# Performance work log

Hardware: AMD Instinct MI355X
Metric: run time of the kernel (lower is better)

The kernel has to match this reference:

```python
import jax, jax.numpy as jnp
import numpy as np

D = 1024
H = 16
HD = D // H
MLP = 4 * D
EPS = 1e-5


def layer_norm(x, g, b):
    mu = jnp.mean(x, axis=-1, keepdims=True)
    var = jnp.mean((x - mu) ** 2, axis=-1, keepdims=True)
    return (x - mu) * jax.lax.rsqrt(var + EPS) * g + b


def grn(stacked, W, b, g, be):
    # stacked: [B, L, S, D]; input-dependent weights + normalized branch, summed over L
    w = jax.nn.relu(jnp.einsum('blsd,de->blse', stacked, W) + b)
    n = layer_norm(stacked, g, be)
    return jnp.sum(w + n, axis=1)  # [B, S, D]


def setup_inputs() -> dict:
    key = jax.random.key(0)
    ks = jax.random.split(key, 24)
    s = 0.02
    inp = {
        'x': jax.random.normal(ks[0], (2, 2048, D), jnp.float32),
        'layer_outputs': jax.random.normal(ks[1], (2, 4, 2048, D), jnp.float32),
    }
    i = 2
    for name in ('q', 'k', 'v'):
        inp[f'grn_{name}_W'] = jax.random.normal(ks[i], (D, D), jnp.float32) * s; i += 1
        inp[f'grn_{name}_b'] = jnp.zeros((D,), jnp.float32)
        inp[f'grn_{name}_g'] = jnp.ones((D,), jnp.float32)
        inp[f'grn_{name}_be'] = jnp.zeros((D,), jnp.float32)
    inp['attn_out_W'] = jax.random.normal(ks[i], (D, D), jnp.float32) * s; i += 1
    inp['attn_out_b'] = jnp.zeros((D,), jnp.float32)
    inp['attn_norm_g'] = jnp.ones((D,), jnp.float32)
    inp['attn_norm_b'] = jnp.zeros((D,), jnp.float32)
    inp['ffn_W1'] = jax.random.normal(ks[i], (D, MLP), jnp.float32) * s; i += 1
    inp['ffn_b1'] = jnp.zeros((MLP,), jnp.float32)
    inp['ffn_W2'] = jax.random.normal(ks[i], (MLP, D), jnp.float32) * s; i += 1
    inp['ffn_b2'] = jnp.zeros((D,), jnp.float32)
    inp['ffn_norm_g'] = jnp.ones((D,), jnp.float32)
    inp['ffn_norm_b'] = jnp.zeros((D,), jnp.float32)
    return inp


def reference(x, layer_outputs,
              grn_q_W, grn_q_b, grn_q_g, grn_q_be,
              grn_k_W, grn_k_b, grn_k_g, grn_k_be,
              grn_v_W, grn_v_b, grn_v_g, grn_v_be,
              attn_out_W, attn_out_b, attn_norm_g, attn_norm_b,
              ffn_W1, ffn_b1, ffn_W2, ffn_b2, ffn_norm_g, ffn_norm_b):
    B, S, _ = x.shape
    q = grn(layer_outputs, grn_q_W, grn_q_b, grn_q_g, grn_q_be)
    k = grn(layer_outputs, grn_k_W, grn_k_b, grn_k_g, grn_k_be)
    v = grn(layer_outputs, grn_v_W, grn_v_b, grn_v_g, grn_v_be)
    # [B, H, S, HD]
    q = q.reshape(B, S, H, HD).transpose(0, 2, 1, 3)
    k = k.reshape(B, S, H, HD).transpose(0, 2, 1, 3)
    v = v.reshape(B, S, H, HD).transpose(0, 2, 1, 3)
    scale = HD ** -0.5
    attn = jnp.einsum('bhqd,bhkd->bhqk', q, k) * scale
    attn = jax.nn.softmax(attn, axis=-1)
    out = jnp.einsum('bhqk,bhkd->bhqd', attn, v)
    out = out.transpose(0, 2, 1, 3).reshape(B, S, D)
    out = out @ attn_out_W + attn_out_b
    out = x + layer_norm(out, attn_norm_g, attn_norm_b)
    h = jax.nn.gelu(out @ ffn_W1 + ffn_b1, approximate=False) @ ffn_W2 + ffn_b2
    out = out + layer_norm(h, ffn_norm_g, ffn_norm_b)
    return out
```

## Files before the change

kernel.cpp:

```cpp
#include <hip/hip_runtime.h>
#include <cstddef>

#define B_  2
#define S_  2048
#define D_  1024
#define L_  4
#define H_  16
#define HD_ 64
#define MLP_ 4096
#define EPS_ 1e-5f

typedef __attribute__((ext_vector_type(8))) short  bf16x8;
typedef __attribute__((ext_vector_type(4))) float  f32x4;

__device__ __forceinline__ unsigned short f2bf(float x) {
    unsigned int u = __float_as_uint(x);
    u = (u + 0x7fffu + ((u >> 16) & 1u)) >> 16;
    return (unsigned short)u;
}
__device__ __forceinline__ float bf2f(unsigned short h) {
    return __uint_as_float(((unsigned int)h) << 16);
}

__global__ __launch_bounds__(256) void wconv_kernel(
    const float* __restrict__ W, unsigned short* __restrict__ Thi,
    unsigned short* __restrict__ Tlo, int K, int N)
{
    __shared__ float T[32][33];
    const int n0 = blockIdx.x * 32, k0 = blockIdx.y * 32;
    const int t = threadIdx.x;
    {
        const int r = t >> 3, c4 = (t & 7) * 4;
        const float4 w = *(const float4*)(W + (size_t)(k0 + r) * N + n0 + c4);
        T[r][c4 + 0] = w.x; T[r][c4 + 1] = w.y;
        T[r][c4 + 2] = w.z; T[r][c4 + 3] = w.w;
    }
    __syncthreads();
    {
        const int n = t >> 3, k4 = (t & 7) * 4;
        ushort4 h, l;
        float f;
        f = T[k4 + 0][n]; h.x = f2bf(f); l.x = f2bf(f - bf2f(h.x));
        f = T[k4 + 1][n]; h.y = f2bf(f); l.y = f2bf(f - bf2f(h.y));
        f = T[k4 + 2][n]; h.z = f2bf(f); l.z = f2bf(f - bf2f(h.z));
        f = T[k4 + 3][n]; h.w = f2bf(f); l.w = f2bf(f - bf2f(h.w));
        *(ushort4*)(Thi + (size_t)(n0 + n) * K + k0 + k4) = h;
        *(ushort4*)(Tlo + (size_t)(n0 + n) * K + k0 + k4) = l;
    }
}

template <int EPI>
__global__ __launch_bounds__(256) void gemm_bf16s_kernel(
    const float* __restrict__ A,
    const unsigned short* __restrict__ Bth, const unsigned short* __restrict__ Btl,
    const float* __restrict__ bias, float* __restrict__ C,
    int M, int N, int K)
{
    __shared__ unsigned short As_hi[128 * 40];
    __shared__ unsigned short As_lo[128 * 40];
    __shared__ unsigned short Bs_hi[128 * 40];
    __shared__ unsigned short Bs_lo[128 * 40];

    const int tid  = threadIdx.x;
    const int lane = tid & 63;
    const int wid  = tid >> 6;
    const int wr   = wid >> 1, wc = wid & 1;
    const int l15  = lane & 15, chunk = lane >> 4;
    const int row0 = blockIdx.y * 128;
    const int col0 = blockIdx.x * 128;

    const int a_off = (wr * 64 + l15) * 40 + chunk * 8;
    const int b_off = (wc * 64 + l15) * 40 + chunk * 8;

    f32x4 acc[4][4] = {};

    for (int k0 = 0; k0 < K; k0 += 32) {
        __syncthreads();
        #pragma unroll
        for (int u = 0; u < 4; ++u) {
            const int idx = tid + u * 256;
            const int r  = idx >> 3;
            const int kc = (idx & 7) * 4;
            const float4 a = *(const float4*)(A + (size_t)(row0 + r) * K + k0 + kc);
            ushort4 h, l;
            h.x = f2bf(a.x); l.x = f2bf(a.x - bf2f(h.x));
            h.y = f2bf(a.y); l.y = f2bf(a.y - bf2f(h.y));
            h.z = f2bf(a.z); l.z = f2bf(a.z - bf2f(h.z));
            h.w = f2bf(a.w); l.w = f2bf(a.w - bf2f(h.w));
            *(ushort4*)&As_hi[r * 40 + kc] = h;
            *(ushort4*)&As_lo[r * 40 + kc] = l;
        }
        #pragma unroll
        for (int u = 0; u < 2; ++u) {
            const int idx = tid + u * 256;
            const int c  = idx >> 2;
            const int kc = (idx & 3) * 8;
            const size_t gb = (size_t)(col0 + c) * K + k0 + kc;
            *(uint4*)&Bs_hi[c * 40 + kc] = *(const uint4*)(Bth + gb);
            *(uint4*)&Bs_lo[c * 40 + kc] = *(const uint4*)(Btl + gb);
        }
        __syncthreads();

        bf16x8 ah[4], al[4], bh[4], bl[4];
        #pragma unroll
        for (int mi = 0; mi < 4; ++mi) {
            ah[mi] = *(const bf16x8*)&As_hi[a_off + mi * 640];
            al[mi] = *(const bf16x8*)&As_lo[a_off + mi * 640];
        }
        #pragma unroll
        for (int ni = 0; ni < 4; ++ni) {
            bh[ni] = *(const bf16x8*)&Bs_hi[b_off + ni * 640];
            bl[ni] = *(const bf16x8*)&Bs_lo[b_off + ni * 640];
        }
        #pragma unroll
        for (int mi = 0; mi < 4; ++mi)
            #pragma unroll
            for (int ni = 0; ni < 4; ++ni) {
                acc[mi][ni] = __builtin_amdgcn_mfma_f32_16x16x32_bf16(
                    ah[mi], bh[ni], acc[mi][ni], 0, 0, 0);
                acc[mi][ni] = __builtin_amdgcn_mfma_f32_16x16x32_bf16(
                    ah[mi], bl[ni], acc[mi][ni], 0, 0, 0);
                acc[mi][ni] = __builtin_amdgcn_mfma_f32_16x16x32_bf16(
                    al[mi], bh[ni], acc[mi][ni], 0, 0, 0);
            }
    }

    const int rbase = row0 + wr * 64 + (lane >> 4) * 4;
    const int cbase = col0 + wc * 64 + l15;
    #pragma unroll
    for (int mi = 0; mi < 4; ++mi) {
        #pragma unroll
        for (int reg = 0; reg < 4; ++reg) {
            const int gr = rbase + mi * 16 + reg;
            #pragma unroll
            for (int ni = 0; ni < 4; ++ni) {
                const int gc = cbase + ni * 16;
                float v = acc[mi][ni][reg] + bias[gc];
                if (EPI == 1) v = fmaxf(v, 0.f);
                else if (EPI == 2) v = 0.5f * v * (1.f + erff(v * 0.70710678118654752f));
                C[(size_t)gr * N + gc] = v;
            }
        }
    }
}

__global__ __launch_bounds__(256) void grn_ns_kernel(
    const float* __restrict__ LO, float* __restrict__ NS)
{
    const int row = blockIdx.x;
    const int b = row >> 11, s = row & (S_ - 1);
    const int tid = threadIdx.x;
    __shared__ float r1[4], r2[4];

    float acc[4] = {0.f, 0.f, 0.f, 0.f};
    #pragma unroll
    for (int l = 0; l < L_; ++l) {
        const float* xr = LO + ((size_t)((b * L_ + l) * S_ + s)) * D_;
        const float4 v = *(const float4*)(xr + tid * 4);
        float s1 = v.x + v.y + v.z + v.w;
        float s2 = v.x * v.x + v.y * v.y + v.z * v.z + v.w * v.w;
        #pragma unroll
        for (int off = 32; off >= 1; off >>= 1) {
            s1 += __shfl_xor(s1, off);
            s2 += __shfl_xor(s2, off);
        }
        if ((tid & 63) == 0) { r1[tid >> 6] = s1; r2[tid >> 6] = s2; }
        __syncthreads();
        s1 = r1[0] + r1[1] + r1[2] + r1[3];
        s2 = r2[0] + r2[1] + r2[2] + r2[3];
        __syncthreads();
        const float mu  = s1 * (1.f / D_);
        const float var = s2 * (1.f / D_) - mu * mu;
        const float rs  = rsqrtf(var + EPS_);
        acc[0] += (v.x - mu) * rs;
        acc[1] += (v.y - mu) * rs;
        acc[2] += (v.z - mu) * rs;
        acc[3] += (v.w - mu) * rs;
    }
    float4 o = {acc[0], acc[1], acc[2], acc[3]};
    *(float4*)(NS + (size_t)row * D_ + tid * 4) = o;
}

__global__ __launch_bounds__(256) void grn_reduce_kernel(
    const float* __restrict__ P, const float* __restrict__ NS,
    const float* __restrict__ g, const float* __restrict__ be,
    float* __restrict__ out)
{
    const size_t i4 = (size_t)blockIdx.x * 256 + threadIdx.x;
    const int d4 = (int)(i4 & (D_ / 4 - 1));
    const size_t row = i4 >> 8;
    const int b = (int)(row >> 11), s = (int)(row & (S_ - 1));

    float4 a = {0.f, 0.f, 0.f, 0.f};
    #pragma unroll
    for (int l = 0; l < L_; ++l) {
        const float4 w = *(const float4*)(P + ((size_t)((b * L_ + l) * S_ + s)) * D_ + d4 * 4);
        a.x += w.x; a.y += w.y; a.z += w.z; a.w += w.w;
    }
    const float4 n  = *(const float4*)(NS + row * D_ + d4 * 4);
    const float4 gg = *(const float4*)(g + d4 * 4);
    const float4 bb = *(const float4*)(be + d4 * 4);
    float4 o;
    o.x = a.x + n.x * gg.x + 4.f * bb.x;
    o.y = a.y + n.y * gg.y + 4.f * bb.y;
    o.z = a.z + n.z * gg.z + 4.f * bb.z;
    o.w = a.w + n.w * gg.w + 4.f * bb.w;
    *(float4*)(out + row * D_ + d4 * 4) = o;
}

__global__ __launch_bounds__(256) void kvconv_kernel(
    const float* __restrict__ Kin, const float* __restrict__ Vin,
    unsigned short* __restrict__ Kh, unsigned short* __restrict__ Kl,
    unsigned short* __restrict__ Vth, unsigned short* __restrict__ Vtl)
{
    __shared__ float T[64][68];
    const int t = threadIdx.x;
    const int st = blockIdx.x;
    const int bh = blockIdx.y;
    const int b = bh >> 4, h = bh & 15;
    const int s0 = st * 64;

    #pragma unroll
    for (int u = 0; u < 4; ++u) {
        const int idx = t + u * 256;
        const int r  = idx >> 4;
        const int c4 = (idx & 15) * 4;
        const size_t src = ((size_t)(b * S_ + s0 + r)) * D_ + h * 64 + c4;
        const float4 kf = *(const float4*)(Kin + src);
        ushort4 hh, ll;
        hh.x = f2bf(kf.x); ll.x = f2bf(kf.x - bf2f(hh.x));
        hh.y = f2bf(kf.y); ll.y = f2bf(kf.y - bf2f(hh.y));
        hh.z = f2bf(kf.z); ll.z = f2bf(kf.z - bf2f(hh.z));
        hh.w = f2bf(kf.w); ll.w = f2bf(kf.w - bf2f(hh.w));
        const size_t kd = ((size_t)bh * S_ + s0 + r) * 64 + c4;
        *(ushort4*)(Kh + kd) = hh;
        *(ushort4*)(Kl + kd) = ll;
        const float4 vf = *(const float4*)(Vin + src);
        T[r][c4 + 0] = vf.x; T[r][c4 + 1] = vf.y;
        T[r][c4 + 2] = vf.z; T[r][c4 + 3] = vf.w;
    }
    __syncthreads();
    #pragma unroll
    for (int u = 0; u < 4; ++u) {
        const int idx = t + u * 256;
        const int d  = idx >> 4;
        const int s4 = (idx & 15) * 4;
        ushort4 hh, ll;
        float f;
        f = T[s4 + 0][d]; hh.x = f2bf(f); ll.x = f2bf(f - bf2f(hh.x));
        f = T[s4 + 1][d]; hh.y = f2bf(f); ll.y = f2bf(f - bf2f(hh.y));
        f = T[s4 + 2][d]; hh.z = f2bf(f); ll.z = f2bf(f - bf2f(hh.z));
        f = T[s4 + 3][d]; hh.w = f2bf(f); ll.w = f2bf(f - bf2f(hh.w));
        const size_t vd = ((size_t)bh * 64 + d) * S_ + s0 + s4;
        *(ushort4*)(Vth + vd) = hh;
        *(ushort4*)(Vtl + vd) = ll;
    }
}

__global__ __launch_bounds__(256) void attn_mfma_kernel(
    const float* __restrict__ Q,
    const unsigned short* __restrict__ Kh, const unsigned short* __restrict__ Kl,
    const unsigned short* __restrict__ Vth, const unsigned short* __restrict__ Vtl,
    float* __restrict__ O)
{
    __shared__ unsigned short Ksh[64 * 72], Ksl[64 * 72];
    __shared__ unsigned short Vsh[64 * 72], Vsl[64 * 72];
    __shared__ unsigned short Phs[4][32 * 72];
    __shared__ unsigned short Pls[4][32 * 72];

    const int tid  = threadIdx.x;
    const int lane = tid & 63;
    const int w    = tid >> 6;
    const int l15  = lane & 15, g = lane >> 4;
    const int bh   = blockIdx.y;
    const int b    = bh >> 4, h = bh & 15;
    const int q0   = blockIdx.x * 128 + w * 32;
    const float scale = 0.125f;

    bf16x8 qh[2][2], ql[2][2];
    #pragma unroll
    for (int mi = 0; mi < 2; ++mi)
        #pragma unroll
        for (int ks = 0; ks < 2; ++ks) {
            const float* qp = Q + ((size_t)(b * S_ + q0 + mi * 16 + l15)) * D_
                              + h * 64 + ks * 32 + g * 8;
            const float4 f0 = *(const float4*)qp;
            const float4 f1 = *(const float4*)(qp + 4);
            const float vs[8] = {f0.x * scale, f0.y * scale, f0.z * scale, f0.w * scale,
                                 f1.x * scale, f1.y * scale, f1.z * scale, f1.w * scale};
            #pragma unroll
            for (int j = 0; j < 8; ++j) {
                const unsigned short hv = f2bf(vs[j]);
                qh[mi][ks][j] = (short)hv;
                ql[mi][ks][j] = (short)f2bf(vs[j] - bf2f(hv));
            }
        }

    f32x4 o[2][4] = {};
    float mrun[2][4], lrun[2][4];
    #pragma unroll
    for (int mi = 0; mi < 2; ++mi)
        #pragma unroll
        for (int r = 0; r < 4; ++r) { mrun[mi][r] = -1e30f; lrun[mi][r] = 0.f; }

    const unsigned short* KhB = Kh  + (size_t)bh * S_ * 64;
    const unsigned short* KlB = Kl  + (size_t)bh * S_ * 64;
    const unsigned short* VhB = Vth + (size_t)bh * 64 * S_;
    const unsigned short* VlB = Vtl + (size_t)bh * 64 * S_;

    for (int kt = 0; kt < S_; kt += 64) {
        __syncthreads();
        #pragma unroll
        for (int u = 0; u < 2; ++u) {
            const int idx = tid + u * 256;
            const int rr  = idx >> 3;
            const int c8  = (idx & 7) * 8;
            *(uint4*)&Ksh[rr * 72 + c8] = *(const uint4*)(KhB + (size_t)(kt + rr) * 64 + c8);
            *(uint4*)&Ksl[rr * 72 + c8] = *(const uint4*)(KlB + (size_t)(kt + rr) * 64 + c8);
            *(uint4*)&Vsh[rr * 72 + c8] = *(const uint4*)(VhB + (size_t)rr * S_ + kt + c8);
            *(uint4*)&Vsl[rr * 72 + c8] = *(const uint4*)(VlB + (size_t)rr * S_ + kt + c8);
        }
        __syncthreads();

        f32x4 s[2][4] = {};
        #pragma unroll
        for (int ks = 0; ks < 2; ++ks)
            #pragma unroll
            for (int ni = 0; ni < 4; ++ni) {
                const bf16x8 khf = *(const bf16x8*)&Ksh[(ni * 16 + l15) * 72 + ks * 32 + g * 8];
                const bf16x8 klf = *(const bf16x8*)&Ksl[(ni * 16 + l15) * 72 + ks * 32 + g * 8];
                #pragma unroll
                for (int mi = 0; mi < 2; ++mi) {
                    s[mi][ni] = __builtin_amdgcn_mfma_f32_16x16x32_bf16(qh[mi][ks], khf, s[mi][ni], 0, 0, 0);
                    s[mi][ni] = __builtin_amdgcn_mfma_f32_16x16x32_bf16(qh[mi][ks], klf, s[mi][ni], 0, 0, 0);
                    s[mi][ni] = __builtin_amdgcn_mfma_f32_16x16x32_bf16(ql[mi][ks], khf, s[mi][ni], 0, 0, 0);
                }
            }

        #pragma unroll
        for (int mi = 0; mi < 2; ++mi) {
            #pragma unroll
            for (int r = 0; r < 4; ++r) {
                float mx = fmaxf(fmaxf(s[mi][0][r], s[mi][1][r]),
                                 fmaxf(s[mi][2][r], s[mi][3][r]));
                mx = fmaxf(mx, __shfl_xor(mx, 1));
                mx = fmaxf(mx, __shfl_xor(mx, 2));
                mx = fmaxf(mx, __shfl_xor(mx, 4));
                mx = fmaxf(mx, __shfl_xor(mx, 8));
                const float mn = fmaxf(mrun[mi][r], mx);
                const float c  = __expf(mrun[mi][r] - mn);
                mrun[mi][r] = mn;
                float rs = 0.f;
                #pragma unroll
                for (int ni = 0; ni < 4; ++ni) {
                    const float p = __expf(s[mi][ni][r] - mn);
                    rs += p;
                    const unsigned short ph = f2bf(p);
                    const int off = (mi * 16 + 4 * g + r) * 72 + ni * 16 + l15;
                    Phs[w][off] = ph;
                    Pls[w][off] = f2bf(p - bf2f(ph));
                }
                rs += __shfl_xor(rs, 1);
                rs += __shfl_xor(rs, 2);
                rs += __shfl_xor(rs, 4);
                rs += __shfl_xor(rs, 8);
                lrun[mi][r] = lrun[mi][r] * c + rs;
                #pragma unroll
                for (int di = 0; di < 4; ++di) o[mi][di][r] *= c;
            }
        }

        #pragma unroll
        for (int ks = 0; ks < 2; ++ks) {
            bf16x8 pfh[2], pfl[2];
            #pragma unroll
            for (int mi = 0; mi < 2; ++mi) {
                pfh[mi] = *(const bf16x8*)&Phs[w][(mi * 16 + l15) * 72 + ks * 32 + g * 8];
                pfl[mi] = *(const bf16x8*)&Pls[w][(mi * 16 + l15) * 72 + ks * 32 + g * 8];
            }
            #pragma unroll
            for (int di = 0; di < 4; ++di) {
                const bf16x8 vhf = *(const bf16x8*)&Vsh[(di * 16 + l15) * 72 + ks * 32 + g * 8];
                const bf16x8 vlf = *(const bf16x8*)&Vsl[(di * 16 + l15) * 72 + ks * 32 + g * 8];
                #pragma unroll
                for (int mi = 0; mi < 2; ++mi) {
                    o[mi][di] = __builtin_amdgcn_mfma_f32_16x16x32_bf16(pfh[mi], vhf, o[mi][di], 0, 0, 0);
                    o[mi][di] = __builtin_amdgcn_mfma_f32_16x16x32_bf16(pfh[mi], vlf, o[mi][di], 0, 0, 0);
                    o[mi][di] = __builtin_amdgcn_mfma_f32_16x16x32_bf16(pfl[mi], vhf, o[mi][di], 0, 0, 0);
                }
            }
        }
    }

    #pragma unroll
    for (int mi = 0; mi < 2; ++mi)
        #pragma unroll
        for (int r = 0; r < 4; ++r) {
            const float inv = 1.f / lrun[mi][r];
            float* op = O + ((size_t)(b * S_ + q0 + mi * 16 + 4 * g + r)) * D_
                        + h * 64 + l15;
            #pragma unroll
            for (int di = 0; di < 4; ++di) op[di * 16] = o[mi][di][r] * inv;
        }
}

__global__ __launch_bounds__(256) void add_ln_kernel(
    const float* __restrict__ Y, const float* __restrict__ R,
    const float* __restrict__ g, const float* __restrict__ beta,
    float* __restrict__ out)
{
    const int row = blockIdx.x;
    const int tid = threadIdx.x;
    __shared__ float r1[4], r2[4];

    const float4 v = *(const float4*)(Y + (size_t)row * D_ + tid * 4);
    float s1 = v.x + v.y + v.z + v.w;
    float s2 = v.x * v.x + v.y * v.y + v.z * v.z + v.w * v.w;
    #pragma unroll
    for (int off = 32; off >= 1; off >>= 1) {
        s1 += __shfl_xor(s1, off);
        s2 += __shfl_xor(s2, off);
    }
    if ((tid & 63) == 0) { r1[tid >> 6] = s1; r2[tid >> 6] = s2; }
    __syncthreads();
    s1 = r1[0] + r1[1] + r1[2] + r1[3];
    s2 = r2[0] + r2[1] + r2[2] + r2[3];
    const float mu  = s1 * (1.f / D_);
    const float var = s2 * (1.f / D_) - mu * mu;
    const float rs  = rsqrtf(var + EPS_);

    const float4 rr = *(const float4*)(R + (size_t)row * D_ + tid * 4);
    const float4 gg = *(const float4*)(g + tid * 4);
    const float4 bb = *(const float4*)(beta + tid * 4);
    float4 o;
    o.x = rr.x + (v.x - mu) * rs * gg.x + bb.x;
    o.y = rr.y + (v.y - mu) * rs * gg.y + bb.y;
    o.z = rr.z + (v.z - mu) * rs * gg.z + bb.z;
    o.w = rr.w + (v.w - mu) * rs * gg.w + bb.w;
    *(float4*)(out + (size_t)row * D_ + tid * 4) = o;
}

extern "C" void kernel_launch(void* const* d_in, const int* in_sizes, int n_in,
                              void* d_out, int out_size, void* d_ws, size_t ws_size,
                              hipStream_t stream)
{
    const float* x  = (const float*)d_in[0];
    const float* LO = (const float*)d_in[1];
    const float* Wq  = (const float*)d_in[2];
    const float* bq_ = (const float*)d_in[3];
    const float* gq  = (const float*)d_in[4];
    const float* beq = (const float*)d_in[5];
    const float* Wk  = (const float*)d_in[6];
    const float* bk_ = (const float*)d_in[7];
    const float* gk  = (const float*)d_in[8];
    const float* bek = (const float*)d_in[9];
    const float* Wv  = (const float*)d_in[10];
    const float* bv_ = (const float*)d_in[11];
    const float* gv  = (const float*)d_in[12];
    const float* bev = (const float*)d_in[13];
    const float* Wo  = (const float*)d_in[14];
    const float* bo  = (const float*)d_in[15];
    const float* ang = (const float*)d_in[16];
    const float* anb = (const float*)d_in[17];
    const float* W1  = (const float*)d_in[18];
    const float* b1  = (const float*)d_in[19];
    const float* W2  = (const float*)d_in[20];
    const float* b2  = (const float*)d_in[21];
    const float* fng = (const float*)d_in[22];
    const float* fnb = (const float*)d_in[23];

    const size_t BS  = (size_t)B_ * S_;
    const size_t SEG = BS * D_;
    float* ws  = (float*)d_ws;
    float* ns   = ws;
    float* bufq = ws + SEG;
    float* bufk = ws + 2 * SEG;
    float* bufv = ws + 3 * SEG;
    float* big  = ws + 4 * SEG;

    unsigned short* wt = (unsigned short*)(ws + 8 * SEG);
    const size_t MM = 1048576;
    unsigned short* wtq_h = wt;            unsigned short* wtq_l = wt + MM;
    unsigned short* wtk_h = wt + 2 * MM;   unsigned short* wtk_l = wt + 3 * MM;
    unsigned short* wtv_h = wt + 4 * MM;   unsigned short* wtv_l = wt + 5 * MM;
    unsigned short* wto_h = wt + 6 * MM;   unsigned short* wto_l = wt + 7 * MM;
    unsigned short* w1_h  = wt + 8 * MM;   unsigned short* w1_l  = wt + 12 * MM;
    unsigned short* w2_h  = wt + 16 * MM;  unsigned short* w2_l  = wt + 20 * MM;

    const size_t KVSEG = (size_t)B_ * H_ * S_ * HD_;
    unsigned short* kv  = (unsigned short*)big;
    unsigned short* kh_ = kv;
    unsigned short* kl_ = kv + KVSEG;
    unsigned short* vth = kv + 2 * KVSEG;
    unsigned short* vtl = kv + 3 * KVSEG;

    const dim3 blk(256);

    wconv_kernel<<<dim3(32, 32),  blk, 0, stream>>>(Wq, wtq_h, wtq_l, D_, D_);
    wconv_kernel<<<dim3(32, 32),  blk, 0, stream>>>(Wk, wtk_h, wtk_l, D_, D_);
    wconv_kernel<<<dim3(32, 32),  blk, 0, stream>>>(Wv, wtv_h, wtv_l, D_, D_);
    wconv_kernel<<<dim3(32, 32),  blk, 0, stream>>>(Wo, wto_h, wto_l, D_, D_);
    wconv_kernel<<<dim3(128, 32), blk, 0, stream>>>(W1, w1_h,  w1_l,  D_, MLP_);
    wconv_kernel<<<dim3(32, 128), blk, 0, stream>>>(W2, w2_h,  w2_l,  MLP_, D_);

    grn_ns_kernel<<<dim3(BS), blk, 0, stream>>>(LO, ns);

    const unsigned short* Wh[3] = {wtq_h, wtk_h, wtv_h};
    const unsigned short* Wl[3] = {wtq_l, wtk_l, wtv_l};
    const float* bp[3]  = {bq_, bk_, bv_};
    const float* gp[3]  = {gq, gk, gv};
    const float* bep[3] = {beq, bek, bev};
    float* outp[3] = {bufq, bufk, bufv};
    for (int p = 0; p < 3; ++p) {
        gemm_bf16s_kernel<1><<<dim3(D_ / 128, (B_ * L_ * S_) / 128), blk, 0, stream>>>(
            LO, Wh[p], Wl[p], bp[p], big, B_ * L_ * S_, D_, D_);
        grn_reduce_kernel<<<dim3(BS), blk, 0, stream>>>(big, ns, gp[p], bep[p], outp[p]);
    }

    kvconv_kernel<<<dim3(S_ / 64, B_ * H_), blk, 0, stream>>>(bufk, bufv, kh_, kl_, vth, vtl);
    attn_mfma_kernel<<<dim3(S_ / 128, B_ * H_), blk, 0, stream>>>(bufq, kh_, kl_, vth, vtl, ns);

    gemm_bf16s_kernel<0><<<dim3(D_ / 128, BS / 128), blk, 0, stream>>>(
        ns, wto_h, wto_l, bo, bufq, (int)BS, D_, D_);

    add_ln_kernel<<<dim3(BS), blk, 0, stream>>>(bufq, x, ang, anb, bufk);

    gemm_bf16s_kernel<2><<<dim3(MLP_ / 128, BS / 128), blk, 0, stream>>>(
        bufk, w1_h, w1_l, b1, big, (int)BS, MLP_, D_);

    gemm_bf16s_kernel<0><<<dim3(D_ / 128, BS / 128), blk, 0, stream>>>(
        big, w2_h, w2_l, b2, bufv, (int)BS, D_, MLP_);

    add_ln_kernel<<<dim3(BS), blk, 0, stream>>>(bufv, bufk, fng, fnb, (float*)d_out);
}
```

Measured before the change: 1.223 ms.

## Pre-split GEMM activations into bf16 hi/lo and drop P low part in attention

Adds a pass that converts fp32 activations into bf16 hi/lo pairs once, plus a GEMM variant that loads these pre-split operands straight into LDS, so each tile no longer splits A on the fly. The FFN1 GEMM now writes its GELU output already split for FFN2. Attention drops the low-order bf16 term of the softmax probabilities, removing one of three MFMAs in the PV product and one LDS buffer. MFMA sections are wrapped in s_setprio. The split layer_outputs path runs only if the workspace is large enough. Dropping the P low term lowers attention accuracy.

```diff
diff --git a/kernel.cpp b/kernel.cpp
--- a/kernel.cpp
+++ b/kernel.cpp
@@ -20,6 +20,21 @@
 }
 __device__ __forceinline__ float bf2f(unsigned short h) {
     return __uint_as_float(((unsigned int)h) << 16);
+}
+
+__global__ __launch_bounds__(256) void aconv_kernel(
+    const float* __restrict__ X, unsigned short* __restrict__ Xh,
+    unsigned short* __restrict__ Xl)
+{
+    const size_t i4 = (size_t)blockIdx.x * 256 + threadIdx.x;
+    const float4 v = *(const float4*)(X + i4 * 4);
+    ushort4 h, l;
+    h.x = f2bf(v.x); l.x = f2bf(v.x - bf2f(h.x));
+    h.y = f2bf(v.y); l.y = f2bf(v.y - bf2f(h.y));
+    h.z = f2bf(v.z); l.z = f2bf(v.z - bf2f(h.z));
+    h.w = f2bf(v.w); l.w = f2bf(v.w - bf2f(h.w));
+    *(ushort4*)(Xh + i4 * 4) = h;
+    *(ushort4*)(Xl + i4 * 4) = l;
 }
 
 __global__ __launch_bounds__(256) void wconv_kernel(
@@ -46,6 +61,99 @@
         f = T[k4 + 3][n]; h.w = f2bf(f); l.w = f2bf(f - bf2f(h.w));
         *(ushort4*)(Thi + (size_t)(n0 + n) * K + k0 + k4) = h;
         *(ushort4*)(Tlo + (size_t)(n0 + n) * K + k0 + k4) = l;
+    }
+}
+
+template <int EPI, int OUT>
+__global__ __launch_bounds__(256) void gemm_bf16p_kernel(
+    const unsigned short* __restrict__ Ah, const unsigned short* __restrict__ Al,
+    const unsigned short* __restrict__ Bth, const unsigned short* __restrict__ Btl,
+    const float* __restrict__ bias, float* __restrict__ C,
+    unsigned short* __restrict__ Chi, unsigned short* __restrict__ Clo,
+    int M, int N, int K)
+{
+    __shared__ unsigned short As_hi[128 * 40];
+    __shared__ unsigned short As_lo[128 * 40];
+    __shared__ unsigned short Bs_hi[128 * 40];
+    __shared__ unsigned short Bs_lo[128 * 40];
+
+    const int tid  = threadIdx.x;
+    const int lane = tid & 63;
+    const int wid  = tid >> 6;
+    const int wr   = wid >> 1, wc = wid & 1;
+    const int l15  = lane & 15, chunk = lane >> 4;
+    const int row0 = blockIdx.y * 128;
+    const int col0 = blockIdx.x * 128;
+
+    const int a_off = (wr * 64 + l15) * 40 + chunk * 8;
+    const int b_off = (wc * 64 + l15) * 40 + chunk * 8;
+
+    f32x4 acc[4][4] = {};
+
+    for (int k0 = 0; k0 < K; k0 += 32) {
+        __syncthreads();
+        #pragma unroll
+        for (int u = 0; u < 2; ++u) {
+            const int idx = tid + u * 256;
+            const int r  = idx >> 2;
+            const int kc = (idx & 3) * 8;
+            const size_t ga = (size_t)(row0 + r) * K + k0 + kc;
+            *(uint4*)&As_hi[r * 40 + kc] = *(const uint4*)(Ah + ga);
+            *(uint4*)&As_lo[r * 40 + kc] = *(const uint4*)(Al + ga);
+            const size_t gb = (size_t)(col0 + r) * K + k0 + kc;
+            *(uint4*)&Bs_hi[r * 40 + kc] = *(const uint4*)(Bth + gb);
+            *(uint4*)&Bs_lo[r * 40 + kc] = *(const uint4*)(Btl + gb);
+        }
+        __syncthreads();
+
+        bf16x8 ah[4], al[4], bh[4], bl[4];
+        #pragma unroll
+        for (int mi = 0; mi < 4; ++mi) {
+            ah[mi] = *(const bf16x8*)&As_hi[a_off + mi * 640];
+            al[mi] = *(const bf16x8*)&As_lo[a_off + mi * 640];
+        }
+        #pragma unroll
+        for (int ni = 0; ni < 4; ++ni) {
+            bh[ni] = *(const bf16x8*)&Bs_hi[b_off + ni * 640];
+            bl[ni] = *(const bf16x8*)&Bs_lo[b_off + ni * 640];
+        }
+        __builtin_amdgcn_s_setprio(1);
+        #pragma unroll
+        for (int mi = 0; mi < 4; ++mi)
+            #pragma unroll
+            for (int ni = 0; ni < 4; ++ni) {
+                acc[mi][ni] = __builtin_amdgcn_mfma_f32_16x16x32_bf16(
+                    ah[mi], bh[ni], acc[mi][ni], 0, 0, 0);
+                acc[mi][ni] = __builtin_amdgcn_mfma_f32_16x16x32_bf16(
+                    ah[mi], bl[ni], acc[mi][ni], 0, 0, 0);
+                acc[mi][ni] = __builtin_amdgcn_mfma_f32_16x16x32_bf16(
+                    al[mi], bh[ni], acc[mi][ni], 0, 0, 0);
+            }
+        __builtin_amdgcn_s_setprio(0);
+    }
+
+    const int rbase = row0 + wr * 64 + (lane >> 4) * 4;
+    const int cbase = col0 + wc * 64 + l15;
+    #pragma unroll
+    for (int mi = 0; mi < 4; ++mi) {
+        #pragma unroll
+        for (int reg = 0; reg < 4; ++reg) {
+            const int gr = rbase + mi * 16 + reg;
+            #pragma unroll
+            for (int ni = 0; ni < 4; ++ni) {
+                const int gc = cbase + ni * 16;
+                float v = acc[mi][ni][reg] + bias[gc];
+                if (EPI == 1) v = fmaxf(v, 0.f);
+                else if (EPI == 2) v = 0.5f * v * (1.f + erff(v * 0.70710678118654752f));
+                if (OUT == 0) {
+                    C[(size_t)gr * N + gc] = v;
+                } else {
+                    const unsigned short hv = f2bf(v);
+                    Chi[(size_t)gr * N + gc] = hv;
+                    Clo[(size_t)gr * N + gc] = f2bf(v - bf2f(hv));
+                }
+            }
+        }
     }
 }
 
@@ -266,7 +374,6 @@
     __shared__ unsigned short Ksh[64 * 72], Ksl[64 * 72];
     __shared__ unsigned short Vsh[64 * 72], Vsl[64 * 72];
     __shared__ unsigned short Phs[4][32 * 72];
-    __shared__ unsigned short Pls[4][32 * 72];
 
     const int tid  = threadIdx.x;
     const int lane = tid & 63;
@@ -329,12 +436,14 @@
             for (int ni = 0; ni < 4; ++ni) {
                 const bf16x8 khf = *(const bf16x8*)&Ksh[(ni * 16 + l15) * 72 + ks * 32 + g * 8];
                 const bf16x8 klf = *(const bf16x8*)&Ksl[(ni * 16 + l15) * 72 + ks * 32 + g * 8];
+                __builtin_amdgcn_s_setprio(1);
                 #pragma unroll
                 for (int mi = 0; mi < 2; ++mi) {
                     s[mi][ni] = __builtin_amdgcn_mfma_f32_16x16x32_bf16(qh[mi][ks], khf, s[mi][ni], 0, 0, 0);
                     s[mi][ni] = __builtin_amdgcn_mfma_f32_16x16x32_bf16(qh[mi][ks], klf, s[mi][ni], 0, 0, 0);
                     s[mi][ni] = __builtin_amdgcn_mfma_f32_16x16x32_bf16(ql[mi][ks], khf, s[mi][ni], 0, 0, 0);
                 }
+                __builtin_amdgcn_s_setprio(0);
             }
 
         #pragma unroll
@@ -355,10 +464,7 @@
                 for (int ni = 0; ni < 4; ++ni) {
                     const float p = __expf(s[mi][ni][r] - mn);
                     rs += p;
-                    const unsigned short ph = f2bf(p);
-                    const int off = (mi * 16 + 4 * g + r) * 72 + ni * 16 + l15;
-                    Phs[w][off] = ph;
-                    Pls[w][off] = f2bf(p - bf2f(ph));
+                    Phs[w][(mi * 16 + 4 * g + r) * 72 + ni * 16 + l15] = f2bf(p);
                 }
                 rs += __shfl_xor(rs, 1);
                 rs += __shfl_xor(rs, 2);
@@ -372,22 +478,21 @@
 
         #pragma unroll
         for (int ks = 0; ks < 2; ++ks) {
-            bf16x8 pfh[2], pfl[2];
-            #pragma unroll
-            for (int mi = 0; mi < 2; ++mi) {
+            bf16x8 pfh[2];
+            #pragma unroll
+            for (int mi = 0; mi < 2; ++mi)
                 pfh[mi] = *(const bf16x8*)&Phs[w][(mi * 16 + l15) * 72 + ks * 32 + g * 8];
-                pfl[mi] = *(const bf16x8*)&Pls[w][(mi * 16 + l15) * 72 + ks * 32 + g * 8];
-            }
             #pragma unroll
             for (int di = 0; di < 4; ++di) {
                 const bf16x8 vhf = *(const bf16x8*)&Vsh[(di * 16 + l15) * 72 + ks * 32 + g * 8];
                 const bf16x8 vlf = *(const bf16x8*)&Vsl[(di * 16 + l15) * 72 + ks * 32 + g * 8];
+                __builtin_amdgcn_s_setprio(1);
                 #pragma unroll
                 for (int mi = 0; mi < 2; ++mi) {
                     o[mi][di] = __builtin_amdgcn_mfma_f32_16x16x32_bf16(pfh[mi], vhf, o[mi][di], 0, 0, 0);
                     o[mi][di] = __builtin_amdgcn_mfma_f32_16x16x32_bf16(pfh[mi], vlf, o[mi][di], 0, 0, 0);
-                    o[mi][di] = __builtin_amdgcn_mfma_f32_16x16x32_bf16(pfl[mi], vhf, o[mi][di], 0, 0, 0);
                 }
+                __builtin_amdgcn_s_setprio(0);
             }
         }
     }
@@ -486,6 +591,9 @@
     unsigned short* wto_h = wt + 6 * MM;   unsigned short* wto_l = wt + 7 * MM;
     unsigned short* w1_h  = wt + 8 * MM;   unsigned short* w1_l  = wt + 12 * MM;
     unsigned short* w2_h  = wt + 16 * MM;  unsigned short* w2_l  = wt + 20 * MM;
+    unsigned short* lo_h = wt + 24 * MM;
+    unsigned short* lo_l = lo_h + 16 * MM;
+    const bool useLoSplit = ws_size >= (size_t)252 * 1024 * 1024;
 
     const size_t KVSEG = (size_t)B_ * H_ * S_ * HD_;
     unsigned short* kv  = (unsigned short*)big;
@@ -493,6 +601,12 @@
     unsigned short* kl_ = kv + KVSEG;
     unsigned short* vth = kv + 2 * KVSEG;
     unsigned short* vtl = kv + 3 * KVSEG;
+    unsigned short* hid_h = (unsigned short*)big;
+    unsigned short* hid_l = hid_h + 16 * MM;
+    unsigned short* ns_h = (unsigned short*)bufv;
+    unsigned short* ns_l = ns_h + 4 * MM;
+    unsigned short* r1_h = (unsigned short*)bufq;
+    unsigned short* r1_l = r1_h + 4 * MM;
 
     const dim3 blk(256);
 
@@ -502,6 +616,8 @@
     wconv_kernel<<<dim3(32, 32),  blk, 0, stream>>>(Wo, wto_h, wto_l, D_, D_);
     wconv_kernel<<<dim3(128, 32), blk, 0, stream>>>(W1, w1_h,  w1_l,  D_, MLP_);
     wconv_kernel<<<dim3(32, 128), blk, 0, stream>>>(W2, w2_h,  w2_l,  MLP_, D_);
+    if (useLoSplit)
+        aconv_kernel<<<dim3(16384), blk, 0, stream>>>(LO, lo_h, lo_l);
 
     grn_ns_kernel<<<dim3(BS), blk, 0, stream>>>(LO, ns);
 
@@ -512,24 +628,31 @@
     const float* bep[3] = {beq, bek, bev};
     float* outp[3] = {bufq, bufk, bufv};
     for (int p = 0; p < 3; ++p) {
-        gemm_bf16s_kernel<1><<<dim3(D_ / 128, (B_ * L_ * S_) / 128), blk, 0, stream>>>(
-            LO, Wh[p], Wl[p], bp[p], big, B_ * L_ * S_, D_, D_);
+        if (useLoSplit)
+            gemm_bf16p_kernel<1, 0><<<dim3(D_ / 128, (B_ * L_ * S_) / 128), blk, 0, stream>>>(
+                lo_h, lo_l, Wh[p], Wl[p], bp[p], big, nullptr, nullptr,
+                B_ * L_ * S_, D_, D_);
+        else
+            gemm_bf16s_kernel<1><<<dim3(D_ / 128, (B_ * L_ * S_) / 128), blk, 0, stream>>>(
+                LO, Wh[p], Wl[p], bp[p], big, B_ * L_ * S_, D_, D_);
         grn_reduce_kernel<<<dim3(BS), blk, 0, stream>>>(big, ns, gp[p], bep[p], outp[p]);
     }
 
     kvconv_kernel<<<dim3(S_ / 64, B_ * H_), blk, 0, stream>>>(bufk, bufv, kh_, kl_, vth, vtl);
     attn_mfma_kernel<<<dim3(S_ / 128, B_ * H_), blk, 0, stream>>>(bufq, kh_, kl_, vth, vtl, ns);
 
-    gemm_bf16s_kernel<0><<<dim3(D_ / 128, BS / 128), blk, 0, stream>>>(
-        ns, wto_h, wto_l, bo, bufq, (int)BS, D_, D_);
+    aconv_kernel<<<dim3(4096), blk, 0, stream>>>(ns, ns_h, ns_l);
+    gemm_bf16p_kernel<0, 0><<<dim3(D_ / 128, BS / 128), blk, 0, stream>>>(
+        ns_h, ns_l, wto_h, wto_l, bo, bufq, nullptr, nullptr, (int)BS, D_, D_);
 
     add_ln_kernel<<<dim3(BS), blk, 0, stream>>>(bufq, x, ang, anb, bufk);
 
-    gemm_bf16s_kernel<2><<<dim3(MLP_ / 128, BS / 128), blk, 0, stream>>>(
-        bufk, w1_h, w1_l, b1, big, (int)BS, MLP_, D_);
-
-    gemm_bf16s_kernel<0><<<dim3(D_ / 128, BS / 128), blk, 0, stream>>>(
-        big, w2_h, w2_l, b2, bufv, (int)BS, D_, MLP_);
+    aconv_kernel<<<dim3(4096), blk, 0, stream>>>(bufk, r1_h, r1_l);
+    gemm_bf16p_kernel<2, 1><<<dim3(MLP_ / 128, BS / 128), blk, 0, stream>>>(
+        r1_h, r1_l, w1_h, w1_l, b1, nullptr, hid_h, hid_l, (int)BS, MLP_, D_);
+
+    gemm_bf16p_kernel<0, 0><<<dim3(D_ / 128, BS / 128), blk, 0, stream>>>(
+        hid_h, hid_l, w2_h, w2_l, b2, bufv, nullptr, nullptr, (int)BS, D_, MLP_);
 
     add_ln_kernel<<<dim3(BS), blk, 0, stream>>>(bufv, bufk, fng, fnb, (float*)d_out);
 }
```

Result: slower. 1.268 ms (+3.7%).
